# Kernel optimization log

Measured on AMD Instinct MI355X. Metric: run time of the kernel, lower is better.

The kernel has to match this reference:

```python
import jax, jax.numpy as jnp
import numpy as np

NP, NO, E, IN_DIM, D = 100000, 200000, 500000, 512, 256
EPS = 1e-12  # torch F.normalize default eps


def setup_inputs() -> dict:
    key = jax.random.key(0)
    ks = jax.random.split(key, 12)
    return {
        "feat_prefix": jax.random.normal(ks[0], (NP, IN_DIM), jnp.float32),
        "feat_other": jax.random.normal(ks[1], (NO, IN_DIM), jnp.float32),
        "src": jax.random.randint(ks[2], (E,), 0, NP),
        "dst": jax.random.randint(ks[3], (E,), 0, NO),
        "Wm_p": jax.random.normal(ks[4], (IN_DIM, D), jnp.float32) * 0.02,
        "bm_p": jax.random.normal(ks[5], (D,), jnp.float32) * 0.02,
        "Wm_o": jax.random.normal(ks[6], (IN_DIM, D), jnp.float32) * 0.02,
        "bm_o": jax.random.normal(ks[7], (D,), jnp.float32) * 0.02,
        "W": jax.random.normal(ks[8], (D, D), jnp.float32) * 0.02,
        "bW": jax.random.normal(ks[9], (D,), jnp.float32) * 0.02,
        "a_w": jax.random.normal(ks[10], (2 * D,), jnp.float32) * 0.02,
        "a_b": jax.random.normal(ks[11], (1,), jnp.float32) * 0.02,
    }


def _l2norm(x):
    n = jnp.linalg.norm(x, axis=-1, keepdims=True)
    return x / jnp.maximum(n, EPS)


def reference(feat_prefix, feat_other, src, dst,
              Wm_p, bm_p, Wm_o, bm_o, W, bW, a_w, a_b):
    # FeatureMappingLayer: per-ntype Linear + ReLU
    hp = jax.nn.relu(feat_prefix @ Wm_p + bm_p)   # [NP, D]
    ho = jax.nn.relu(feat_other @ Wm_o + bm_o)    # [NO, D]
    d = hp.shape[1]
    n_prefix = hp.shape[0]

    # GAT-style score: a([W h_src ; W h_dst]) -- project at node level,
    # decompose the concat-linear into two per-node dot products, then gather.
    hp_proj = hp @ W + bW                         # [NP, D]
    ho_proj = ho @ W + bW                         # [NO, D]
    s_src = hp_proj @ a_w[:d]                     # [NP]
    s_dst = ho_proj @ a_w[d:]                     # [NO]
    e = s_src[src] + s_dst[dst] + a_b[0]          # [E] per-edge scores

    # Segment softmax over source (Prefix) node
    m = jax.ops.segment_max(e, src, num_segments=n_prefix)
    m = jnp.where(jnp.isfinite(m), m, 0.0)        # empty segments -> 0
    ex = jnp.exp(e - m[src])
    denom = jax.ops.segment_sum(ex, src, num_segments=n_prefix)
    alpha = ex / denom[src]                       # [E]

    # Scatter-weighted sum of mapped (pre-W) dst features into Prefix nodes
    agg = jax.ops.segment_sum(alpha[:, None] * ho[dst], src,
                              num_segments=n_prefix)  # [NP, D]

    return (_l2norm(agg), _l2norm(ho))
```

## Files before the change

kernel.cpp:

```cpp
#include <hip/hip_runtime.h>
#include <math.h>

#define IN_DIM 512
#define DD 256

typedef _Float16 half8_t __attribute__((ext_vector_type(8)));
typedef _Float16 half4_t __attribute__((ext_vector_type(4)));
typedef __attribute__((ext_vector_type(4))) float f32x4_t;

__global__ __launch_bounds__(256) void prep_w2(const float* __restrict__ W,
                                               const float* __restrict__ a_w,
                                               float* __restrict__ w2) {
  int row = (blockIdx.x * 256 + threadIdx.x) >> 6;
  int lane = threadIdx.x & 63;
  if (row >= DD) return;
  float4 wv = *reinterpret_cast<const float4*>(&W[(size_t)row * DD + lane * 4]);
  float4 av = *reinterpret_cast<const float4*>(&a_w[DD + lane * 4]);
  float s = wv.x * av.x + wv.y * av.y + wv.z * av.z + wv.w * av.w;
#pragma unroll
  for (int d = 32; d; d >>= 1) s += __shfl_xor(s, d, 64);
  if (lane == 0) w2[row] = s;
}

__global__ void bconv_kernel(const float* __restrict__ Wm, _Float16* __restrict__ Bh) {
  int i = blockIdx.x * 256 + threadIdx.x;
  int k = i >> 8, col = i & 255;
  int kc16 = k >> 5, kr = k & 31;
  int lane = ((kr >> 3) << 4) | (col & 15);
  int nf = col >> 4;
  int off = (((((kc16 << 4) + nf) << 6) + lane) << 3) + (kr & 7);
  Bh[off] = (_Float16)Wm[i];
}

__device__ __forceinline__ half8_t cvt8(const float4& a, const float4& b) {
  half8_t h;
  h[0] = (_Float16)a.x; h[1] = (_Float16)a.y; h[2] = (_Float16)a.z; h[3] = (_Float16)a.w;
  h[4] = (_Float16)b.x; h[5] = (_Float16)b.y; h[6] = (_Float16)b.z; h[7] = (_Float16)b.w;
  return h;
}

__global__ __launch_bounds__(256, 2) void map_gemm_mfma(
    const float* __restrict__ X, const _Float16* __restrict__ Bh,
    const float* __restrict__ bm, const float* __restrict__ w2,
    float* __restrict__ Yn, _Float16* __restrict__ Y16,
    float* __restrict__ wnorm, int M) {
  __shared__ ushort Ah[2][8192];
  const int t = threadIdx.x;
  const int w = t >> 6;
  const int l = t & 63;
  const int c = l & 15;
  const int g = l >> 4;
  const int row0 = blockIdx.x * 64;

  const int sr = t >> 2;
  const int skb = (t & 3) << 5;
  int gr = row0 + sr;
  if (gr >= M) gr = M - 1;
  const float* xrow = X + (size_t)gr * IN_DIM;

  f32x4_t acc[4][4];
#pragma unroll
  for (int m = 0; m < 4; ++m)
#pragma unroll
    for (int n = 0; n < 4; ++n) acc[m][n] = (f32x4_t){0.f, 0.f, 0.f, 0.f};

  const int sw = (sr & 15) << 3;
  const int i0 = (sr << 7) + skb;
  const half8_t* bhb = reinterpret_cast<const half8_t*>(Bh);

  float4 st[2][8];
  {
    const float4* p0 = reinterpret_cast<const float4*>(xrow + skb);
    const float4* p1 = reinterpret_cast<const float4*>(xrow + 128 + skb);
#pragma unroll
    for (int i = 0; i < 8; ++i) st[0][i] = p0[i];
#pragma unroll
    for (int i = 0; i < 8; ++i) st[1][i] = p1[i];
    *reinterpret_cast<half8_t*>(&Ah[0][(i0 + 0) ^ sw]) = cvt8(st[0][0], st[0][1]);
    *reinterpret_cast<half8_t*>(&Ah[0][(i0 + 8) ^ sw]) = cvt8(st[0][2], st[0][3]);
    *reinterpret_cast<half8_t*>(&Ah[0][(i0 + 16) ^ sw]) = cvt8(st[0][4], st[0][5]);
    *reinterpret_cast<half8_t*>(&Ah[0][(i0 + 24) ^ sw]) = cvt8(st[0][6], st[0][7]);
  }
  __syncthreads();

#pragma unroll
  for (int ks = 0; ks < 4; ++ks) {
    const int cur = ks & 1;
    if (ks < 2) {
      const float4* p = reinterpret_cast<const float4*>(xrow + ((ks + 2) << 7) + skb);
#pragma unroll
      for (int i = 0; i < 8; ++i) st[ks & 1][i] = p[i];
    }

#pragma unroll
    for (int kc = 0; kc < 4; ++kc) {
      const int kc16 = (ks << 2) + kc;
      half8_t ah[4];
#pragma unroll
      for (int m = 0; m < 4; ++m) {
        int r = (m << 4) + c;
        int idx = ((r << 7) + (kc << 5) + (g << 3)) ^ (c << 3);
        ah[m] = *reinterpret_cast<const half8_t*>(&Ah[cur][idx]);
      }
      half8_t bh[4];
#pragma unroll
      for (int n = 0; n < 4; ++n)
        bh[n] = bhb[(((kc16 << 4) + (w << 2) + n) << 6) + l];
#pragma unroll
      for (int n = 0; n < 4; ++n)
#pragma unroll
        for (int m = 0; m < 4; ++m)
          acc[m][n] = __builtin_amdgcn_mfma_f32_16x16x32_f16(ah[m], bh[n], acc[m][n], 0, 0, 0);
    }

    if (ks < 3) {
      const int nxt = cur ^ 1;
      const int sidx = (ks + 1) & 1;
      *reinterpret_cast<half8_t*>(&Ah[nxt][(i0 + 0) ^ sw]) = cvt8(st[sidx][0], st[sidx][1]);
      *reinterpret_cast<half8_t*>(&Ah[nxt][(i0 + 8) ^ sw]) = cvt8(st[sidx][2], st[sidx][3]);
      *reinterpret_cast<half8_t*>(&Ah[nxt][(i0 + 16) ^ sw]) = cvt8(st[sidx][4], st[sidx][5]);
      *reinterpret_cast<half8_t*>(&Ah[nxt][(i0 + 24) ^ sw]) = cvt8(st[sidx][6], st[sidx][7]);
    }
    __syncthreads();
  }

  float bv[4], wv[4];
#pragma unroll
  for (int n = 0; n < 4; ++n) {
    bv[n] = bm[(w << 6) + (n << 4) + c];
    wv[n] = w2[(w << 6) + (n << 4) + c];
  }
#pragma unroll
  for (int m = 0; m < 4; ++m)
#pragma unroll
    for (int n = 0; n < 4; ++n)
#pragma unroll
      for (int q = 0; q < 4; ++q) {
        float v = acc[m][n][q] + bv[n];
        acc[m][n][q] = v > 0.f ? v : 0.f;
      }

  float* red = reinterpret_cast<float*>(&Ah[0][0]);
  float pss[4][4], pdt[4][4];
#pragma unroll
  for (int m = 0; m < 4; ++m)
#pragma unroll
    for (int q = 0; q < 4; ++q) {
      float ss = 0.f, dt = 0.f;
#pragma unroll
      for (int n = 0; n < 4; ++n) {
        float a = acc[m][n][q];
        ss = fmaf(a, a, ss);
        dt = fmaf(a, wv[n], dt);
      }
      for (int d = 8; d; d >>= 1) {
        ss += __shfl_down(ss, d, 16);
        dt += __shfl_down(dt, d, 16);
      }
      pss[m][q] = ss;
      pdt[m][q] = dt;
    }
  __syncthreads();
#pragma unroll
  for (int m = 0; m < 4; ++m)
#pragma unroll
    for (int q = 0; q < 4; ++q)
      if (c == 0) {
        int rr = (m << 4) + (g << 2) + q;
        red[(w << 6) + rr] = pss[m][q];
        red[256 + (w << 6) + rr] = pdt[m][q];
      }
  __syncthreads();
  if (t < 64) {
    float ss = red[t] + red[64 + t] + red[128 + t] + red[192 + t];
    float dt = red[256 + t] + red[320 + t] + red[384 + t] + red[448 + t];
    float nr = sqrtf(ss);
    red[512 + t] = 1.f / fmaxf(nr, 1e-12f);
    int r = row0 + t;
    if (r < M) wnorm[r] = expf(dt) * nr;
  }
  __syncthreads();
#pragma unroll
  for (int m = 0; m < 4; ++m)
#pragma unroll
    for (int q = 0; q < 4; ++q) {
      int rr = (m << 4) + (g << 2) + q;
      float sc = red[512 + rr];
      int r = row0 + rr;
      if (r < M) {
#pragma unroll
        for (int n = 0; n < 4; ++n) {
          float v = acc[m][n][q] * sc;
          int col = (w << 6) + (n << 4) + c;
          Yn[(size_t)r * DD + col] = v;
          Y16[(size_t)r * DD + col] = (_Float16)v;
        }
      }
    }
}

__global__ void hist_kernel(const int* __restrict__ src, int* __restrict__ deg, int E) {
  int i = blockIdx.x * blockDim.x + threadIdx.x;
  if (i < E) atomicAdd(&deg[src[i]], 1);
}

__global__ __launch_bounds__(256) void scan_part(const int* __restrict__ deg,
                                                 int* __restrict__ bsum, int NP) {
  __shared__ int s[256];
  int t = threadIdx.x, b = blockIdx.x;
  int i0 = (b * 256 + t) * 2;
  int v0 = (i0 < NP) ? deg[i0] : 0;
  int v1 = (i0 + 1 < NP) ? deg[i0 + 1] : 0;
  s[t] = v0 + v1;
  __syncthreads();
  for (int off = 128; off; off >>= 1) {
    if (t < off) s[t] += s[t + off];
    __syncthreads();
  }
  if (t == 0) bsum[b] = s[0];
}

__global__ __launch_bounds__(256) void scan_top(int* __restrict__ bsum,
                                                int* __restrict__ rowptr_last) {
  __shared__ int s[256];
  int t = threadIdx.x;
  int v = bsum[t];
  s[t] = v;
  __syncthreads();
  for (int off = 1; off < 256; off <<= 1) {
    int u = (t >= off) ? s[t - off] : 0;
    __syncthreads();
    s[t] += u;
    __syncthreads();
  }
  bsum[t] = s[t] - v;
  if (t == 255) *rowptr_last = s[255];
}

__global__ __launch_bounds__(256) void scan_fin(const int* __restrict__ deg,
                                                const int* __restrict__ bsum,
                                                int* __restrict__ rowptr,
                                                int* __restrict__ cursor, int NP) {
  __shared__ int s[256];
  int t = threadIdx.x, b = blockIdx.x;
  int i0 = (b * 256 + t) * 2;
  int v0 = (i0 < NP) ? deg[i0] : 0;
  int v1 = (i0 + 1 < NP) ? deg[i0 + 1] : 0;
  int local = v0 + v1;
  s[t] = local;
  __syncthreads();
  for (int off = 1; off < 256; off <<= 1) {
    int u = (t >= off) ? s[t - off] : 0;
    __syncthreads();
    s[t] += u;
    __syncthreads();
  }
  int base = bsum[b] + s[t] - local;
  if (i0 < NP) { rowptr[i0] = base; cursor[i0] = base; }
  if (i0 + 1 < NP) { rowptr[i0 + 1] = base + v0; cursor[i0 + 1] = base + v0; }
}

__global__ void fill_kernel(const int* __restrict__ src, const int* __restrict__ dst,
                            int* __restrict__ cursor, int* __restrict__ ebuf, int E) {
  int i = blockIdx.x * blockDim.x + threadIdx.x;
  if (i < E) {
    int pos = atomicAdd(&cursor[src[i]], 1);
    ebuf[pos] = dst[i];
  }
}

__global__ void agg_kernel(const int* __restrict__ rowptr, const int* __restrict__ ebuf,
                           const float* __restrict__ wnorm, const _Float16* __restrict__ hon16,
                           float* __restrict__ agg, int NP) {
  int p = (int)(((long)blockIdx.x * blockDim.x + threadIdx.x) >> 6);
  int lane = threadIdx.x & 63;
  if (p >= NP) return;
  int beg = rowptr[p], end = rowptr[p + 1];
  float4 acc = {0.f, 0.f, 0.f, 0.f};
  if (beg < end) {
    int d0 = ebuf[beg];
    float w0 = wnorm[d0];
    half4_t v0 = *reinterpret_cast<const half4_t*>(&hon16[(size_t)d0 * DD + lane * 4]);
    float w1 = 0.f;
    half4_t v1 = {0, 0, 0, 0};
    if (beg + 1 < end) {
      int d1 = ebuf[beg + 1];
      w1 = wnorm[d1];
      v1 = *reinterpret_cast<const half4_t*>(&hon16[(size_t)d1 * DD + lane * 4]);
    }
    for (int j = beg; j < end; ++j) {
      float wn_ = 0.f;
      half4_t vn = {0, 0, 0, 0};
      if (j + 2 < end) {
        int dn = ebuf[j + 2];
        wn_ = wnorm[dn];
        vn = *reinterpret_cast<const half4_t*>(&hon16[(size_t)dn * DD + lane * 4]);
      }
      acc.x = fmaf(w0, (float)v0[0], acc.x);
      acc.y = fmaf(w0, (float)v0[1], acc.y);
      acc.z = fmaf(w0, (float)v0[2], acc.z);
      acc.w = fmaf(w0, (float)v0[3], acc.w);
      w0 = w1; v0 = v1; w1 = wn_; v1 = vn;
    }
  }
  float ss = acc.x * acc.x + acc.y * acc.y + acc.z * acc.z + acc.w * acc.w;
#pragma unroll
  for (int d = 32; d > 0; d >>= 1) ss += __shfl_xor(ss, d, 64);
  float inv = 1.0f / fmaxf(sqrtf(ss), 1e-12f);
  float4 o = {acc.x * inv, acc.y * inv, acc.z * inv, acc.w * inv};
  *reinterpret_cast<float4*>(&agg[(size_t)p * DD + lane * 4]) = o;
}

extern "C" void kernel_launch(void* const* d_in, const int* in_sizes, int n_in,
                              void* d_out, int out_size, void* d_ws, size_t ws_size,
                              hipStream_t stream) {
  const float* feat_other = (const float*)d_in[1];
  const int* src = (const int*)d_in[2];
  const int* dst = (const int*)d_in[3];
  const float* Wm_o = (const float*)d_in[6];
  const float* bm_o = (const float*)d_in[7];
  const float* W = (const float*)d_in[8];
  const float* a_w = (const float*)d_in[10];

  const int NP = in_sizes[0] / IN_DIM;
  const int NO = in_sizes[1] / IN_DIM;
  const int E = in_sizes[2];

  float* out = (float*)d_out;
  float* agg_out = out;
  float* ho_out = out + (size_t)NP * DD;

  float* ws = (float*)d_ws;
  float* wnorm = ws;
  float* w2 = wnorm + NO;
  int* deg = (int*)(w2 + 256);
  int* rowptr = deg + NP;
  int* cursor = rowptr + NP + 1;
  int* bsum = cursor + NP;
  int* ebuf = bsum + 256;
  size_t foff = (size_t)NO + 256 + NP + (NP + 1) + NP + 256 + E;
  foff = (foff + 3) & ~(size_t)3;
  _Float16* Bh = (_Float16*)(ws + foff);
  _Float16* Y16 = Bh + (size_t)IN_DIM * DD;

  hipMemsetAsync(deg, 0, (size_t)NP * sizeof(int), stream);

  prep_w2<<<64, 256, 0, stream>>>(W, a_w, w2);
  bconv_kernel<<<(IN_DIM * DD) / 256, 256, 0, stream>>>(Wm_o, Bh);

  map_gemm_mfma<<<(NO + 63) / 64, 256, 0, stream>>>(
      feat_other, Bh, bm_o, w2, ho_out, Y16, wnorm, NO);

  hist_kernel<<<(E + 255) / 256, 256, 0, stream>>>(src, deg, E);
  scan_part<<<256, 256, 0, stream>>>(deg, bsum, NP);
  scan_top<<<1, 256, 0, stream>>>(bsum, rowptr + NP);
  scan_fin<<<256, 256, 0, stream>>>(deg, bsum, rowptr, cursor, NP);
  fill_kernel<<<(E + 255) / 256, 256, 0, stream>>>(src, dst, cursor, ebuf, E);

  agg_kernel<<<(NP * 64 + 255) / 256, 256, 0, stream>>>(
      rowptr, ebuf, wnorm, Y16, agg_out, NP);
}
```

Before: 376.2 us.

## Restructure mapping GEMM so each wave owns full rows, staging B in LDS

The mapping GEMM now gives each wave 16 complete output rows across all 256 columns. A is read straight from global memory into registers, and the shared LDS tile now double-buffers slices of the B matrix instead of A. Because a wave holds whole rows, the row-norm and score reductions stay within the wave as shuffles, removing the cross-wave LDS reduction and its extra barriers. Occupancy is raised to 3 blocks per CU. The trade-off is that each A fragment is reused across only 16 MFMAs, and every block re-reads the full B matrix from global or L2 memory for each K chunk.

```diff
diff --git a/kernel.cpp b/kernel.cpp
--- a/kernel.cpp
+++ b/kernel.cpp
@@ -39,164 +39,105 @@
   return h;
 }
 
-__global__ __launch_bounds__(256, 2) void map_gemm_mfma(
+__global__ __launch_bounds__(256, 3) void map_gemm_mfma(
     const float* __restrict__ X, const _Float16* __restrict__ Bh,
     const float* __restrict__ bm, const float* __restrict__ w2,
     float* __restrict__ Yn, _Float16* __restrict__ Y16,
     float* __restrict__ wnorm, int M) {
-  __shared__ ushort Ah[2][8192];
+  __shared__ _Float16 Bs[2][8192];
   const int t = threadIdx.x;
-  const int w = t >> 6;
   const int l = t & 63;
   const int c = l & 15;
   const int g = l >> 4;
-  const int row0 = blockIdx.x * 64;
-
-  const int sr = t >> 2;
-  const int skb = (t & 3) << 5;
-  int gr = row0 + sr;
-  if (gr >= M) gr = M - 1;
-  const float* xrow = X + (size_t)gr * IN_DIM;
-
-  f32x4_t acc[4][4];
-#pragma unroll
-  for (int m = 0; m < 4; ++m)
-#pragma unroll
-    for (int n = 0; n < 4; ++n) acc[m][n] = (f32x4_t){0.f, 0.f, 0.f, 0.f};
-
-  const int sw = (sr & 15) << 3;
-  const int i0 = (sr << 7) + skb;
-  const half8_t* bhb = reinterpret_cast<const half8_t*>(Bh);
-
-  float4 st[2][8];
+  const int row0 = blockIdx.x * 64 + (t >> 6) * 16;
+
+  int arow = row0 + c;
+  if (arow >= M) arow = M - 1;
+  const float* xrow = X + (size_t)arow * IN_DIM;
+
+  f32x4_t acc[16];
+#pragma unroll
+  for (int n = 0; n < 16; ++n) acc[n] = (f32x4_t){0.f, 0.f, 0.f, 0.f};
+
+  const uint4* bsrc = reinterpret_cast<const uint4*>(Bh);
+
   {
-    const float4* p0 = reinterpret_cast<const float4*>(xrow + skb);
-    const float4* p1 = reinterpret_cast<const float4*>(xrow + 128 + skb);
-#pragma unroll
-    for (int i = 0; i < 8; ++i) st[0][i] = p0[i];
-#pragma unroll
-    for (int i = 0; i < 8; ++i) st[1][i] = p1[i];
-    *reinterpret_cast<half8_t*>(&Ah[0][(i0 + 0) ^ sw]) = cvt8(st[0][0], st[0][1]);
-    *reinterpret_cast<half8_t*>(&Ah[0][(i0 + 8) ^ sw]) = cvt8(st[0][2], st[0][3]);
-    *reinterpret_cast<half8_t*>(&Ah[0][(i0 + 16) ^ sw]) = cvt8(st[0][4], st[0][5]);
-    *reinterpret_cast<half8_t*>(&Ah[0][(i0 + 24) ^ sw]) = cvt8(st[0][6], st[0][7]);
-  }
+    uint4* bd = reinterpret_cast<uint4*>(&Bs[0][0]);
+#pragma unroll
+    for (int j = 0; j < 4; ++j) bd[j * 256 + t] = bsrc[j * 256 + t];
+  }
+  float4 xa = *reinterpret_cast<const float4*>(xrow + g * 8);
+  float4 xb = *reinterpret_cast<const float4*>(xrow + g * 8 + 4);
   __syncthreads();
 
 #pragma unroll
-  for (int ks = 0; ks < 4; ++ks) {
-    const int cur = ks & 1;
-    if (ks < 2) {
-      const float4* p = reinterpret_cast<const float4*>(xrow + ((ks + 2) << 7) + skb);
-#pragma unroll
-      for (int i = 0; i < 8; ++i) st[ks & 1][i] = p[i];
-    }
-
-#pragma unroll
-    for (int kc = 0; kc < 4; ++kc) {
-      const int kc16 = (ks << 2) + kc;
-      half8_t ah[4];
-#pragma unroll
-      for (int m = 0; m < 4; ++m) {
-        int r = (m << 4) + c;
-        int idx = ((r << 7) + (kc << 5) + (g << 3)) ^ (c << 3);
-        ah[m] = *reinterpret_cast<const half8_t*>(&Ah[cur][idx]);
+  for (int kc = 0; kc < 16; ++kc) {
+    const int cur = kc & 1;
+    uint4 s0, s1, s2, s3;
+    float4 nxa, nxb;
+    if (kc < 15) {
+      const int gb = (kc + 1) * 1024 + t;
+      s0 = bsrc[gb]; s1 = bsrc[gb + 256]; s2 = bsrc[gb + 512]; s3 = bsrc[gb + 768];
+      const float* xp = xrow + (kc + 1) * 32 + g * 8;
+      nxa = *reinterpret_cast<const float4*>(xp);
+      nxb = *reinterpret_cast<const float4*>(xp + 4);
+    }
+    half8_t ah = cvt8(xa, xb);
+#pragma unroll
+    for (int n = 0; n < 16; ++n) {
+      half8_t bh = *reinterpret_cast<const half8_t*>(&Bs[cur][n * 512 + l * 8]);
+      acc[n] = __builtin_amdgcn_mfma_f32_16x16x32_f16(ah, bh, acc[n], 0, 0, 0);
+    }
+    if (kc < 15) {
+      uint4* bd = reinterpret_cast<uint4*>(&Bs[cur ^ 1][0]);
+      bd[t] = s0; bd[256 + t] = s1; bd[512 + t] = s2; bd[768 + t] = s3;
+      xa = nxa; xb = nxb;
+    }
+    __syncthreads();
+  }
+
+  float ssq[4] = {0.f, 0.f, 0.f, 0.f}, dtq[4] = {0.f, 0.f, 0.f, 0.f};
+#pragma unroll
+  for (int n = 0; n < 16; ++n) {
+    float bvn = bm[n * 16 + c];
+    float wvn = w2[n * 16 + c];
+#pragma unroll
+    for (int q = 0; q < 4; ++q) {
+      float v = acc[n][q] + bvn;
+      v = v > 0.f ? v : 0.f;
+      acc[n][q] = v;
+      ssq[q] = fmaf(v, v, ssq[q]);
+      dtq[q] = fmaf(v, wvn, dtq[q]);
+    }
+  }
+#pragma unroll
+  for (int q = 0; q < 4; ++q) {
+#pragma unroll
+    for (int d = 1; d < 16; d <<= 1) {
+      ssq[q] += __shfl_xor(ssq[q], d, 16);
+      dtq[q] += __shfl_xor(dtq[q], d, 16);
+    }
+  }
+  float inv[4];
+#pragma unroll
+  for (int q = 0; q < 4; ++q) {
+    float nr = sqrtf(ssq[q]);
+    inv[q] = 1.f / fmaxf(nr, 1e-12f);
+    int r = row0 + g * 4 + q;
+    if (c == 0 && r < M) wnorm[r] = expf(dtq[q]) * nr;
+  }
+#pragma unroll
+  for (int q = 0; q < 4; ++q) {
+    int r = row0 + g * 4 + q;
+    if (r < M) {
+#pragma unroll
+      for (int n = 0; n < 16; ++n) {
+        float v = acc[n][q] * inv[q];
+        Yn[(size_t)r * DD + n * 16 + c] = v;
+        Y16[(size_t)r * DD + n * 16 + c] = (_Float16)v;
       }
-      half8_t bh[4];
-#pragma unroll
-      for (int n = 0; n < 4; ++n)
-        bh[n] = bhb[(((kc16 << 4) + (w << 2) + n) << 6) + l];
-#pragma unroll
-      for (int n = 0; n < 4; ++n)
-#pragma unroll
-        for (int m = 0; m < 4; ++m)
-          acc[m][n] = __builtin_amdgcn_mfma_f32_16x16x32_f16(ah[m], bh[n], acc[m][n], 0, 0, 0);
-    }
-
-    if (ks < 3) {
-      const int nxt = cur ^ 1;
-      const int sidx = (ks + 1) & 1;
-      *reinterpret_cast<half8_t*>(&Ah[nxt][(i0 + 0) ^ sw]) = cvt8(st[sidx][0], st[sidx][1]);
-      *reinterpret_cast<half8_t*>(&Ah[nxt][(i0 + 8) ^ sw]) = cvt8(st[sidx][2], st[sidx][3]);
-      *reinterpret_cast<half8_t*>(&Ah[nxt][(i0 + 16) ^ sw]) = cvt8(st[sidx][4], st[sidx][5]);
-      *reinterpret_cast<half8_t*>(&Ah[nxt][(i0 + 24) ^ sw]) = cvt8(st[sidx][6], st[sidx][7]);
-    }
-    __syncthreads();
-  }
-
-  float bv[4], wv[4];
-#pragma unroll
-  for (int n = 0; n < 4; ++n) {
-    bv[n] = bm[(w << 6) + (n << 4) + c];
-    wv[n] = w2[(w << 6) + (n << 4) + c];
-  }
-#pragma unroll
-  for (int m = 0; m < 4; ++m)
-#pragma unroll
-    for (int n = 0; n < 4; ++n)
-#pragma unroll
-      for (int q = 0; q < 4; ++q) {
-        float v = acc[m][n][q] + bv[n];
-        acc[m][n][q] = v > 0.f ? v : 0.f;
-      }
-
-  float* red = reinterpret_cast<float*>(&Ah[0][0]);
-  float pss[4][4], pdt[4][4];
-#pragma unroll
-  for (int m = 0; m < 4; ++m)
-#pragma unroll
-    for (int q = 0; q < 4; ++q) {
-      float ss = 0.f, dt = 0.f;
-#pragma unroll
-      for (int n = 0; n < 4; ++n) {
-        float a = acc[m][n][q];
-        ss = fmaf(a, a, ss);
-        dt = fmaf(a, wv[n], dt);
-      }
-      for (int d = 8; d; d >>= 1) {
-        ss += __shfl_down(ss, d, 16);
-        dt += __shfl_down(dt, d, 16);
-      }
-      pss[m][q] = ss;
-      pdt[m][q] = dt;
-    }
-  __syncthreads();
-#pragma unroll
-  for (int m = 0; m < 4; ++m)
-#pragma unroll
-    for (int q = 0; q < 4; ++q)
-      if (c == 0) {
-        int rr = (m << 4) + (g << 2) + q;
-        red[(w << 6) + rr] = pss[m][q];
-        red[256 + (w << 6) + rr] = pdt[m][q];
-      }
-  __syncthreads();
-  if (t < 64) {
-    float ss = red[t] + red[64 + t] + red[128 + t] + red[192 + t];
-    float dt = red[256 + t] + red[320 + t] + red[384 + t] + red[448 + t];
-    float nr = sqrtf(ss);
-    red[512 + t] = 1.f / fmaxf(nr, 1e-12f);
-    int r = row0 + t;
-    if (r < M) wnorm[r] = expf(dt) * nr;
-  }
-  __syncthreads();
-#pragma unroll
-  for (int m = 0; m < 4; ++m)
-#pragma unroll
-    for (int q = 0; q < 4; ++q) {
-      int rr = (m << 4) + (g << 2) + q;
-      float sc = red[512 + rr];
-      int r = row0 + rr;
-      if (r < M) {
-#pragma unroll
-        for (int n = 0; n < 4; ++n) {
-          float v = acc[m][n][q] * sc;
-          int col = (w << 6) + (n << 4) + c;
-          Yn[(size_t)r * DD + col] = v;
-          Y16[(size_t)r * DD + col] = (_Float16)v;
-        }
-      }
-    }
+    }
+  }
 }
 
 __global__ void hist_kernel(const int* __restrict__ src, int* __restrict__ deg, int E) {
```

After: 371.8 us. No clear change (-1.2%).
